# Kernel optimization log

Hardware: AMD Instinct MI355X
Metric: run time of the kernel (lower is better)

The kernel has to match this reference:

```python
import jax, jax.numpy as jnp
import numpy as np

WINDOW = 100   # window_size
HEADS = 8      # num_heads
KDIM = 64      # Keras MHA key_dim (= value_dim by default)
D = 512        # model dim (query/key/value feature dim)
B = 8
L = 4096       # not a multiple of WINDOW -> pad_len = 4


def setup_inputs() -> dict:
    key = jax.random.key(0)
    ks = jax.random.split(key, 5)
    s = 0.02  # small init scale like glorot
    return {
        "x":  jax.random.normal(ks[0], (B, L, D), jnp.float32),
        "Wq": jax.random.normal(ks[1], (D, HEADS, KDIM), jnp.float32) * s,
        "bq": jnp.zeros((HEADS, KDIM), jnp.float32),
        "Wk": jax.random.normal(ks[2], (D, HEADS, KDIM), jnp.float32) * s,
        "bk": jnp.zeros((HEADS, KDIM), jnp.float32),
        "Wv": jax.random.normal(ks[3], (D, HEADS, KDIM), jnp.float32) * s,
        "bv": jnp.zeros((HEADS, KDIM), jnp.float32),
        "Wo": jax.random.normal(ks[4], (HEADS, KDIM, D), jnp.float32) * s,
        "bo": jnp.zeros((D,), jnp.float32),
    }


def reference(x, Wq, bq, Wk, bk, Wv, bv, Wo, bo):
    Bx, Lx, Dx = x.shape
    pad_len = (WINDOW - Lx % WINDOW) % WINDOW
    xp = jnp.pad(x, ((0, 0), (0, pad_len), (0, 0)))          # [B, L+pad, D]
    n_win = (Lx + pad_len) // WINDOW
    xw = xp.reshape(Bx * n_win, WINDOW, Dx)                  # [B*N, W, D]

    # Keras MultiHeadAttention(num_heads=HEADS, key_dim=KDIM), self-attention
    q = jnp.einsum('bwd,dhk->bwhk', xw, Wq) + bq             # [B*N, W, H, K]
    k = jnp.einsum('bwd,dhk->bwhk', xw, Wk) + bk
    v = jnp.einsum('bwd,dhk->bwhk', xw, Wv) + bv

    scale = 1.0 / np.sqrt(KDIM).astype(np.float32)
    scores = jnp.einsum('bqhk,bshk->bhqs', q, k) * scale     # [B*N, H, W, W]
    attn = jax.nn.softmax(scores, axis=-1)
    o = jnp.einsum('bhqs,bshk->bqhk', attn, v)               # [B*N, W, H, K]
    y = jnp.einsum('bqhk,hkd->bqd', o, Wo) + bo              # [B*N, W, D]

    return y.reshape(Bx, n_win, WINDOW, Dx)                  # pad_len is static (=4 here)
```

## Files before the change

kernel.cpp:

```cpp
#include <hip/hip_runtime.h>

typedef unsigned short u16;
typedef __attribute__((ext_vector_type(4))) float f32x4;
typedef __attribute__((ext_vector_type(8))) short short8;

#define WIN_SZ 100
#define NWIN 41
#define NBATCH 8
#define SEQ 4096
#define DM 512
#define NHEAD 8
#define KD 64
#define NWINS (NBATCH * NWIN)
#define MROWS (NWINS * WIN_SZ)
#define MBLKS 257
#define TOKPB (NWIN * WIN_SZ)
#define NQKV 1536

#define OFF_XBF   0u
#define OFF_OBUF  16793600u
#define OFF_WQKVT 33587200u
#define OFF_WOT   34373632u
#define OFF_ZBLK  34635776u
#define OFF_BIAS  34636032u
#define OFF_BIAS2 34639104u

__device__ __forceinline__ u16 f2bf(float f) {
  union { float f; unsigned i; } v; v.f = f;
  unsigned r = (v.i + 0x7fffu + ((v.i >> 16) & 1u)) >> 16;
  return (u16)r;
}

__device__ __forceinline__ void gl2lds16(const void* g, void* lds) {
  __builtin_amdgcn_global_load_lds(
      (const __attribute__((address_space(1))) void*)g,
      (__attribute__((address_space(3))) void*)lds, 16, 0, 0);
}

__global__ void prep_k(const float* __restrict__ Wq, const float* __restrict__ Wk,
                       const float* __restrict__ Wv, const float* __restrict__ Wo,
                       const float* __restrict__ bq, const float* __restrict__ bk,
                       const float* __restrict__ bv, const float* __restrict__ bo,
                       u16* __restrict__ ws) {
  __shared__ u16 tile[64][65];
  const int z = blockIdx.z;
  const float* src = (z == 0) ? Wq : (z == 1) ? Wk : (z == 2) ? Wv : Wo;
  u16* dst = (z < 3) ? (ws + OFF_WQKVT + (unsigned)z * 512u * 512u)
                     : (ws + OFF_WOT);
  const int k0 = blockIdx.y * 64, n0 = blockIdx.x * 64;
  const int t = threadIdx.x;
  const int c = t & 63, r4 = t >> 6;
#pragma unroll
  for (int p = 0; p < 16; ++p) {
    int r = p * 4 + r4;
    tile[r][c] = f2bf(src[(size_t)(k0 + r) * 512 + n0 + c]);
  }
  __syncthreads();
#pragma unroll
  for (int p = 0; p < 16; ++p) {
    int r = p * 4 + r4;
    dst[(size_t)(n0 + r) * 512 + k0 + c] = tile[c][r];
  }
  if (blockIdx.x == 0 && blockIdx.y == 0) {
    float* biasF = (float*)(ws + OFF_BIAS);
    float* biasO = (float*)(ws + OFF_BIAS2);
    for (int j = t; j < 512; j += 256) {
      if (z == 0) biasF[j] = bq[j];
      else if (z == 1) biasF[512 + j] = bk[j];
      else if (z == 2) biasF[1024 + j] = bv[j];
      else biasO[j] = bo[j];
    }
    if (z == 3 && t < 128) ws[OFF_ZBLK + t] = 0;
  }
}

__global__ void convx_k(const float* __restrict__ x, u16* __restrict__ ws) {
  u16* xbf = ws + OFF_XBF;
  int i = blockIdx.x * 256 + threadIdx.x;
  if (i >= MROWS * 128) return;
  int m = i >> 7;
  int c4 = (i & 127) * 4;
  int b = m / TOKPB, tk = m - b * TOKPB;
  float4 v = make_float4(0.f, 0.f, 0.f, 0.f);
  if (tk < SEQ) v = *(const float4*)(x + (size_t)(b * SEQ + tk) * DM + c4);
  u16 o[4] = {f2bf(v.x), f2bf(v.y), f2bf(v.z), f2bf(v.w)};
  *(uint2*)(xbf + (size_t)m * DM + c4) = *(const uint2*)o;
}

#define QKS 72
#define PS 136
#define SM_ELEMS 24832

__global__ __launch_bounds__(256, 3)
void qkvattn_k(const u16* __restrict__ ws) {
  __shared__ u16 smem[SM_ELEMS];
  u16* Xs  = smem;
  u16* Wsl = smem + 7168;
  u16* Vt  = smem;
  u16* Qs  = smem + 8704;
  u16* Ks  = smem + 16768;
  u16* P   = smem + 8704;

  const int win = blockIdx.x, h = blockIdx.y;
  const int t = threadIdx.x, w = t >> 6, l = t & 63;
  const int q = l >> 4, cl = l & 15;
  const int lsw = (((t & 7) ^ ((t >> 3) & 7)) * 8);

  unsigned xoff[4];
#pragma unroll
  for (int i = 0; i < 4; ++i) {
    int m = i * 32 + (t >> 3);
    xoff[i] = (m < WIN_SZ)
                  ? (OFF_XBF + (unsigned)(win * WIN_SZ + m) * DM + lsw)
                  : OFF_ZBLK;
  }
  unsigned woff[6];
#pragma unroll
  for (int i = 0; i < 6; ++i) {
    int g = i * 32 + (t >> 3);
    unsigned nrow = (unsigned)(g >> 6) * 512u + (unsigned)h * 64u + (g & 63);
    woff[i] = OFF_WQKVT + nrow * DM + lsw;
  }

  f32x4 acc_p[7][3] = {};
  for (int k0 = 0; k0 < DM; k0 += 64) {
    __syncthreads();
#pragma unroll
    for (int i = 0; i < 4; ++i)
      if (i * 32 + w * 8 < 112)
        gl2lds16(ws + xoff[i] + (xoff[i] == OFF_ZBLK ? 0u : (unsigned)k0),
                 &Xs[(i * 32 + w * 8) * 64]);
#pragma unroll
    for (int i = 0; i < 6; ++i)
      gl2lds16(ws + woff[i] + k0, &Wsl[(i * 32 + w * 8) * 64]);
    __syncthreads();
#pragma unroll
    for (int ks = 0; ks < 2; ++ks) {
      const int ko = ks * 32 + q * 8;
      const int koS = ko ^ ((cl & 7) << 3);
      short8 af[7], bf[3];
#pragma unroll
      for (int mt = 0; mt < 7; ++mt)
        af[mt] = *(const short8*)&Xs[(mt * 16 + cl) * 64 + koS];
#pragma unroll
      for (int ntl = 0; ntl < 3; ++ntl)
        bf[ntl] = *(const short8*)&Wsl[((3 * w + ntl) * 16 + cl) * 64 + koS];
#pragma unroll
      for (int mt = 0; mt < 7; ++mt)
#pragma unroll
        for (int ntl = 0; ntl < 3; ++ntl)
          acc_p[mt][ntl] = __builtin_amdgcn_mfma_f32_16x16x32_bf16(
              af[mt], bf[ntl], acc_p[mt][ntl], 0, 0, 0);
    }
  }
  __syncthreads();

  {
    const float* biasF = (const float*)(ws + OFF_BIAS);
#pragma unroll
    for (int ntl = 0; ntl < 3; ++ntl) {
      const int nt = 3 * w + ntl;
      const int cw = (nt & 3) * 16 + cl;
      const float bb = biasF[(nt >> 2) * 512 + h * 64 + cw];
#pragma unroll
      for (int mt = 0; mt < 7; ++mt)
#pragma unroll
        for (int r = 0; r < 4; ++r) {
          const int tok = mt * 16 + q * 4 + r;
          const u16 v16 = f2bf(acc_p[mt][ntl][r] + bb);
          if (nt < 4) Qs[tok * QKS + cw] = v16;
          else if (nt < 8) Ks[tok * QKS + cw] = v16;
          else Vt[cw * PS + tok] = v16;
        }
    }
    for (int idx = t; idx < 64 * 24; idx += 256)
      Vt[(idx / 24) * PS + 112 + idx % 24] = 0;
  }
  __syncthreads();

  const int nmt = (w < 3) ? 2 : 1;
  const int mt0 = w, mt1 = w + 4;

  f32x4 accs[2][7];
#pragma unroll
  for (int im = 0; im < 2; ++im) {
    if (im < nmt) {
      const int mt = (im == 0) ? mt0 : mt1;
      const int ar = (mt * 16 + cl) * QKS + q * 8;
      short8 a0 = *(const short8*)&Qs[ar];
      short8 a1 = *(const short8*)&Qs[ar + 32];
#pragma unroll
      for (int nt = 0; nt < 7; ++nt) {
        const int br = (nt * 16 + cl) * QKS + q * 8;
        short8 b0 = *(const short8*)&Ks[br];
        short8 b1 = *(const short8*)&Ks[br + 32];
        f32x4 c = {};
        c = __builtin_amdgcn_mfma_f32_16x16x32_bf16(a0, b0, c, 0, 0, 0);
        c = __builtin_amdgcn_mfma_f32_16x16x32_bf16(a1, b1, c, 0, 0, 0);
        accs[im][nt] = c;
      }
    }
  }

  const float scale = 0.125f;
#pragma unroll
  for (int im = 0; im < 2; ++im) {
    if (im < nmt) {
#pragma unroll
      for (int r = 0; r < 4; ++r) {
        float mx = -1e30f;
#pragma unroll
        for (int nt = 0; nt < 7; ++nt) {
          float s = accs[im][nt][r] * scale;
          if ((nt < 6) || (cl < 4)) mx = fmaxf(mx, s);
        }
        mx = fmaxf(mx, __shfl_xor(mx, 1, 64));
        mx = fmaxf(mx, __shfl_xor(mx, 2, 64));
        mx = fmaxf(mx, __shfl_xor(mx, 4, 64));
        mx = fmaxf(mx, __shfl_xor(mx, 8, 64));
        float sum = 0.f;
#pragma unroll
        for (int nt = 0; nt < 7; ++nt) {
          float s = accs[im][nt][r] * scale;
          bool valid = (nt < 6) || (cl < 4);
          float e = valid ? __expf(s - mx) : 0.f;
          accs[im][nt][r] = e;
          sum += e;
        }
        sum += __shfl_xor(sum, 1, 64);
        sum += __shfl_xor(sum, 2, 64);
        sum += __shfl_xor(sum, 4, 64);
        sum += __shfl_xor(sum, 8, 64);
        float inv = 1.0f / sum;
#pragma unroll
        for (int nt = 0; nt < 7; ++nt) accs[im][nt][r] *= inv;
      }
    }
  }
  __syncthreads();

#pragma unroll
  for (int im = 0; im < 2; ++im) {
    if (im < nmt) {
      const int mt = (im == 0) ? mt0 : mt1;
#pragma unroll
      for (int nt = 0; nt < 7; ++nt)
#pragma unroll
        for (int r = 0; r < 4; ++r)
          P[(mt * 16 + q * 4 + r) * PS + nt * 16 + cl] = f2bf(accs[im][nt][r]);
    }
  }
  for (int idx = t; idx < 112 * 24; idx += 256)
    P[(idx / 24) * PS + 112 + idx % 24] = 0;
  __syncthreads();

  f32x4 acco[2][4] = {};
#pragma unroll
  for (int ks = 0; ks < 4; ++ks) {
    const int ko = ks * 32 + q * 8;
    short8 a0 = *(const short8*)&P[(mt0 * 16 + cl) * PS + ko];
    short8 a1 = a0;
    if (nmt == 2) a1 = *(const short8*)&P[(mt1 * 16 + cl) * PS + ko];
#pragma unroll
    for (int nt = 0; nt < 4; ++nt) {
      short8 b = *(const short8*)&Vt[(nt * 16 + cl) * PS + ko];
      acco[0][nt] = __builtin_amdgcn_mfma_f32_16x16x32_bf16(a0, b, acco[0][nt], 0, 0, 0);
      if (nmt == 2)
        acco[1][nt] = __builtin_amdgcn_mfma_f32_16x16x32_bf16(a1, b, acco[1][nt], 0, 0, 0);
    }
  }

  u16* obuf = (u16*)(ws + OFF_OBUF);
  const size_t orow0 = (size_t)win * WIN_SZ;
#pragma unroll
  for (int im = 0; im < 2; ++im) {
    if (im < nmt) {
      const int mt = (im == 0) ? mt0 : mt1;
#pragma unroll
      for (int nt = 0; nt < 4; ++nt)
#pragma unroll
        for (int r = 0; r < 4; ++r) {
          int row = mt * 16 + q * 4 + r;
          if (row < WIN_SZ)
            obuf[(orow0 + row) * DM + h * KD + nt * 16 + cl] = f2bf(acco[im][nt][r]);
        }
    }
  }
}

__global__ __launch_bounds__(256, 4)
void gemm_k(const u16* __restrict__ ws, unsigned aoff0, unsigned btoff,
            unsigned biasoff, float* __restrict__ Cout, int Ntot) {
  __shared__ u16 Alds[128 * 64];
  __shared__ u16 Blds[128 * 64];

  const int t = threadIdx.x;
  const int w = t >> 6;
  const int l = t & 63;
  const int nb = blockIdx.x, mb = blockIdx.y;
  const int m0 = mb * 128, n0 = nb * 128;
  const int lr = t >> 3;
  const int lsw = (((t & 7) ^ ((t >> 3) & 7)) * 8);

  unsigned aoff[4], boff[4];
#pragma unroll
  for (int i = 0; i < 4; ++i) {
    int m = m0 + i * 32 + lr;
    aoff[i] = (m < MROWS) ? (aoff0 + (unsigned)m * DM + lsw) : OFF_ZBLK;
    boff[i] = btoff + (unsigned)(n0 + i * 32 + lr) * DM + lsw;
  }

  f32x4 acc[4][4] = {};
  const int wm = (w & 1) * 64;
  const int wn = (w >> 1) * 64;
  const int q = l >> 4, cl = l & 15;

  for (int k0 = 0; k0 < DM; k0 += 64) {
    __syncthreads();
#pragma unroll
    for (int i = 0; i < 4; ++i) {
      gl2lds16(ws + aoff[i] + (aoff[i] == OFF_ZBLK ? 0u : (unsigned)k0),
               &Alds[(i * 32 + w * 8) * 64]);
      gl2lds16(ws + boff[i] + k0, &Blds[(i * 32 + w * 8) * 64]);
    }
    __syncthreads();
#pragma unroll
    for (int ks = 0; ks < 2; ++ks) {
      short8 av[4], bv_[4];
      const int ko = ks * 32 + q * 8;
      const int koS = ko ^ ((cl & 7) << 3);
#pragma unroll
      for (int mi = 0; mi < 4; ++mi)
        av[mi] = *(const short8*)&Alds[(wm + mi * 16 + cl) * 64 + koS];
#pragma unroll
      for (int ni = 0; ni < 4; ++ni)
        bv_[ni] = *(const short8*)&Blds[(wn + ni * 16 + cl) * 64 + koS];
#pragma unroll
      for (int mi = 0; mi < 4; ++mi)
#pragma unroll
        for (int ni = 0; ni < 4; ++ni)
          acc[mi][ni] = __builtin_amdgcn_mfma_f32_16x16x32_bf16(
              av[mi], bv_[ni], acc[mi][ni], 0, 0, 0);
    }
  }

  const float* biasF = (const float*)(ws + biasoff);
#pragma unroll
  for (int mi = 0; mi < 4; ++mi) {
#pragma unroll
    for (int ni = 0; ni < 4; ++ni) {
      int col = n0 + wn + ni * 16 + cl;
      float bb = biasF[col];
#pragma unroll
      for (int r = 0; r < 4; ++r) {
        int row = m0 + wm + mi * 16 + q * 4 + r;
        if (row < MROWS)
          Cout[(size_t)row * Ntot + col] = acc[mi][ni][r] + bb;
      }
    }
  }
}

extern "C" void kernel_launch(void* const* d_in, const int* in_sizes, int n_in,
                              void* d_out, int out_size, void* d_ws, size_t ws_size,
                              hipStream_t stream) {
  const float* x  = (const float*)d_in[0];
  const float* Wq = (const float*)d_in[1];
  const float* bq = (const float*)d_in[2];
  const float* Wk = (const float*)d_in[3];
  const float* bk = (const float*)d_in[4];
  const float* Wv = (const float*)d_in[5];
  const float* bv = (const float*)d_in[6];
  const float* Wo = (const float*)d_in[7];
  const float* bo = (const float*)d_in[8];

  u16* ws = (u16*)d_ws;

  prep_k<<<dim3(8, 8, 4), dim3(256), 0, stream>>>(
      Wq, Wk, Wv, Wo, bq, bk, bv, bo, ws);
  convx_k<<<dim3((MROWS * 128 + 255) / 256), dim3(256), 0, stream>>>(x, ws);
  qkvattn_k<<<dim3(NWINS, NHEAD), dim3(256), 0, stream>>>(ws);
  gemm_k<<<dim3(DM / 128, MBLKS), dim3(256), 0, stream>>>(
      ws, OFF_OBUF, OFF_WOT, OFF_BIAS2, (float*)d_out, DM);
}
```

Baseline: 277.9 us.

## Double-buffer X and weight tiles in QKV projection loop

Converts the K-loop of the QKV projection into a two-stage pipeline: the next 64-wide slice of X and weights is issued into a second LDS buffer while MFMAs run on the current one. This removes one barrier per iteration and lets global loads overlap compute. LDS use roughly doubles, so launch bounds drop from 3 to 2 blocks per SM, which lowers occupancy. The async gl2lds copies are only ordered by the end-of-iteration barrier, so correctness depends on that wait covering them.

New measurement: 287.2 us. 3.3% more time.

```diff
diff --git a/kernel.cpp b/kernel.cpp
--- a/kernel.cpp
+++ b/kernel.cpp
@@ -89,13 +89,12 @@
 
 #define QKS 72
 #define PS 136
-#define SM_ELEMS 24832
-
-__global__ __launch_bounds__(256, 3)
+#define SM_ELEMS 38912
+#define STG_BUF 19456
+
+__global__ __launch_bounds__(256, 2)
 void qkvattn_k(const u16* __restrict__ ws) {
   __shared__ u16 smem[SM_ELEMS];
-  u16* Xs  = smem;
-  u16* Wsl = smem + 7168;
   u16* Vt  = smem;
   u16* Qs  = smem + 8704;
   u16* Ks  = smem + 16768;
@@ -123,17 +122,32 @@
   }
 
   f32x4 acc_p[7][3] = {};
-  for (int k0 = 0; k0 < DM; k0 += 64) {
-    __syncthreads();
-#pragma unroll
-    for (int i = 0; i < 4; ++i)
-      if (i * 32 + w * 8 < 112)
-        gl2lds16(ws + xoff[i] + (xoff[i] == OFF_ZBLK ? 0u : (unsigned)k0),
-                 &Xs[(i * 32 + w * 8) * 64]);
-#pragma unroll
-    for (int i = 0; i < 6; ++i)
-      gl2lds16(ws + woff[i] + k0, &Wsl[(i * 32 + w * 8) * 64]);
-    __syncthreads();
+
+#pragma unroll
+  for (int i = 0; i < 4; ++i)
+    if (i * 32 + w * 8 < 112)
+      gl2lds16(ws + xoff[i], &smem[(i * 32 + w * 8) * 64]);
+#pragma unroll
+  for (int i = 0; i < 6; ++i)
+    gl2lds16(ws + woff[i], &smem[7168 + (i * 32 + w * 8) * 64]);
+  __syncthreads();
+
+  for (int it = 0; it < 8; ++it) {
+    const int cur = it & 1;
+    if (it < 7) {
+      const unsigned k0n = (unsigned)(it + 1) * 64u;
+      const unsigned bb = (unsigned)(cur ^ 1) * STG_BUF;
+#pragma unroll
+      for (int i = 0; i < 4; ++i)
+        if (i * 32 + w * 8 < 112)
+          gl2lds16(ws + xoff[i] + (xoff[i] == OFF_ZBLK ? 0u : k0n),
+                   &smem[bb + (i * 32 + w * 8) * 64]);
+#pragma unroll
+      for (int i = 0; i < 6; ++i)
+        gl2lds16(ws + woff[i] + k0n, &smem[bb + 7168 + (i * 32 + w * 8) * 64]);
+    }
+    const u16* Xb = smem + cur * STG_BUF;
+    const u16* Wb = Xb + 7168;
 #pragma unroll
     for (int ks = 0; ks < 2; ++ks) {
       const int ko = ks * 32 + q * 8;
@@ -141,10 +155,10 @@
       short8 af[7], bf[3];
 #pragma unroll
       for (int mt = 0; mt < 7; ++mt)
-        af[mt] = *(const short8*)&Xs[(mt * 16 + cl) * 64 + koS];
+        af[mt] = *(const short8*)&Xb[(mt * 16 + cl) * 64 + koS];
 #pragma unroll
       for (int ntl = 0; ntl < 3; ++ntl)
-        bf[ntl] = *(const short8*)&Wsl[((3 * w + ntl) * 16 + cl) * 64 + koS];
+        bf[ntl] = *(const short8*)&Wb[((3 * w + ntl) * 16 + cl) * 64 + koS];
 #pragma unroll
       for (int mt = 0; mt < 7; ++mt)
 #pragma unroll
@@ -152,8 +166,8 @@
           acc_p[mt][ntl] = __builtin_amdgcn_mfma_f32_16x16x32_bf16(
               af[mt], bf[ntl], acc_p[mt][ntl], 0, 0, 0);
     }
-  }
-  __syncthreads();
+    __syncthreads();
+  }
 
   {
     const float* biasF = (const float*)(ws + OFF_BIAS);
```
